# Optimization experiments

Measured on AMD Instinct MI355X. Metric: run time of the kernel, lower is better.

Reference implementation:

```python
import jax, jax.numpy as jnp
import numpy as np

STDDEV = 0.1  # matches Regularizer(stddev=0.1)


def setup_inputs() -> dict:
    key = jax.random.key(0)
    k1, k2, k3, k4 = jax.random.split(key, 4)
    B, S, D = 2048, 256, 128  # batch, num_samples, n_input
    return {
        "x": jax.random.normal(k1, (B, D), dtype=jnp.float32),
        "noise": jax.random.normal(k2, (B, S, D), dtype=jnp.float32),
        "W": jax.random.normal(k3, (D, 1), dtype=jnp.float32) * 0.1,  # inner model weight
        "b": jax.random.normal(k4, (1,), dtype=jnp.float32),          # inner model bias
    }


def reference(x, noise, W, b):
    B, S, D = noise.shape
    # neighborhood: x repeated + Gaussian noise, plus constant column -> [B, S, D+1]
    xl_feat = x[:, None, :] + noise * STDDEV                      # [B, S, D]
    ones = jnp.ones((B, S, 1), dtype=x.dtype)
    xl = jnp.concatenate([xl_feat, ones], axis=-1)                # [B, S, D+1]

    # inner model (linear + sigmoid classifier) evaluated on the neighborhood
    y = jax.nn.sigmoid(xl_feat @ W + b)                           # [B, S, 1]

    # local least-squares fit: Beta = (X^T X)^{-1} X^T y, batched over B
    XtX = jnp.einsum('bsi,bsj->bij', xl, xl)                      # [B, D+1, D+1]
    Xty = jnp.einsum('bsi,bsk->bik', xl, y)                       # [B, D+1, 1]
    Beta = jnp.linalg.solve(XtX, Xty)                             # [B, D+1, 1]

    # linear predictions -> sigmoid -> BCE(target = model output)
    y_lin = jnp.einsum('bsi,bik->bsk', xl, Beta)                  # [B, S, 1]
    logp = jax.nn.log_sigmoid(y_lin)
    log1mp = jax.nn.log_sigmoid(-y_lin)
    bce = -(y * logp + (1.0 - y) * log1mp)                        # [B, S, 1]
    # mean over stacked per-sample BCE means == global mean (equal sizes)
    return jnp.mean(bce)
```

## Files before the change

### kernel.cpp

```cpp
#include <hip/hip_runtime.h>
#include <math.h>

#define NB 2048
#define NS 256
#define ND 128
#define NCOL 129
#define LDA 132
#define TS 32
#define XTP 40
#define BSTRIDE 132
#define STDDEV 0.1f

typedef __attribute__((ext_vector_type(8))) short bf16x8;
typedef __attribute__((ext_vector_type(4))) float f32x4;

__device__ inline unsigned short f32_to_bf16_rn(float f) {
  unsigned int u = __float_as_uint(f);
  unsigned int r = (u + 0x7FFFu + ((u >> 16) & 1u)) >> 16;
  return (unsigned short)r;
}
__device__ inline float bf16u_to_f32(unsigned short h) {
  return __uint_as_float(((unsigned int)h) << 16);
}
__device__ inline float rdlane(float v, int lane) {
  return __int_as_float(__builtin_amdgcn_readlane(__float_as_int(v), lane));
}

#define FOR_ROW(F, i) F(i,0) F(i,1) F(i,2) F(i,3) F(i,4) F(i,5) F(i,6) F(i,7)
#define FOR_ALL(F) FOR_ROW(F,0) FOR_ROW(F,1) FOR_ROW(F,2) FOR_ROW(F,3) \
                   FOR_ROW(F,4) FOR_ROW(F,5) FOR_ROW(F,6) FOR_ROW(F,7)

#define ACC_DECL(i,j) float a##i##_##j = 0.f;
#define ACC_UPD(i,j)  a##i##_##j = fmaf(-m##i, rc##j, a##i##_##j);

#define ACC8(cc, c, m) \
  a##cc##_0 = fmaf(-(m), a##c##_0, a##cc##_0); \
  a##cc##_1 = fmaf(-(m), a##c##_1, a##cc##_1); \
  a##cc##_2 = fmaf(-(m), a##c##_2, a##cc##_2); \
  a##cc##_3 = fmaf(-(m), a##c##_3, a##cc##_3); \
  a##cc##_4 = fmaf(-(m), a##c##_4, a##cc##_4); \
  a##cc##_5 = fmaf(-(m), a##c##_5, a##cc##_5); \
  a##cc##_6 = fmaf(-(m), a##c##_6, a##cc##_6); \
  a##cc##_7 = fmaf(-(m), a##c##_7, a##cc##_7);

#define PF_U(c, cc) { const float m_ = pv##cc * pinv; \
  ACC8(cc, c, m_) \
  rh##cc = fmaf(-m_, rh##c, rh##cc); \
  bc##cc = fmaf(-m_, bc##c, bc##cc); }

#define PF_STEP(c, J0, J1, J2, J3, UPDS) { \
  const float pv0 = rdlane(a##c##_##J0, lsrc0); \
  const float pv1 = rdlane(a##c##_##J1, lsrc0); \
  const float pv2 = rdlane(a##c##_##J2, lsrc0); \
  const float pv3 = rdlane(a##c##_##J3, lsrc0); \
  const float pv4 = rdlane(a##c##_##J0, lsrc1); \
  const float pv5 = rdlane(a##c##_##J1, lsrc1); \
  const float pv6 = rdlane(a##c##_##J2, lsrc1); \
  const float pv7 = rdlane(a##c##_##J3, lsrc1); \
  const float pinv = 1.0f / pv##c; \
  if (tx == 3) pdiag[p8 + (c)] = pinv; \
  const float mb_ = bc##c * pinv; \
  cornb = fmaf(-mb_, bc##c, cornb); \
  cornr = fmaf(-mb_, rh##c, cornr); \
  UPDS }

#define PUBROW(c) \
  *(float4*)&rbp[(c) * LDA + txc0] = make_float4(a##c##_0, a##c##_1, a##c##_2, a##c##_3); \
  *(float4*)&rbp[(c) * LDA + txc1] = make_float4(a##c##_4, a##c##_5, a##c##_6, a##c##_7);

#define TRAIL_C(c) { \
  const float4 o0_ = *(const float4*)&rbp[(c) * LDA + ty8]; \
  const float4 o1_ = *(const float4*)&rbp[(c) * LDA + ty8 + 4]; \
  const float4 c0_ = *(const float4*)&rbp[(c) * LDA + txc0]; \
  const float4 c1_ = *(const float4*)&rbp[(c) * LDA + txc1]; \
  const float pk_ = pd[(c)]; \
  const float m0 = o0_.x*pk_, m1 = o0_.y*pk_, m2 = o0_.z*pk_, m3 = o0_.w*pk_; \
  const float m4 = o1_.x*pk_, m5 = o1_.y*pk_, m6 = o1_.z*pk_, m7 = o1_.w*pk_; \
  const float rc0 = c0_.x, rc1 = c0_.y, rc2 = c0_.z, rc3 = c0_.w; \
  const float rc4 = c1_.x, rc5 = c1_.y, rc6 = c1_.z, rc7 = c1_.w; \
  FOR_ALL(ACC_UPD) \
  hr0 = fmaf(m0, rp[(c)], hr0); hr1 = fmaf(m1, rp[(c)], hr1); \
  hr2 = fmaf(m2, rp[(c)], hr2); hr3 = fmaf(m3, rp[(c)], hr3); \
  hr4 = fmaf(m4, rp[(c)], hr4); hr5 = fmaf(m5, rp[(c)], hr5); \
  hr6 = fmaf(m6, rp[(c)], hr6); hr7 = fmaf(m7, rp[(c)], hr7); \
  hb0 = fmaf(m0, bp[(c)], hb0); hb1 = fmaf(m1, bp[(c)], hb1); \
  hb2 = fmaf(m2, bp[(c)], hb2); hb3 = fmaf(m3, bp[(c)], hb3); \
  hb4 = fmaf(m4, bp[(c)], hb4); hb5 = fmaf(m5, bp[(c)], hb5); \
  hb6 = fmaf(m6, bp[(c)], hb6); hb7 = fmaf(m7, bp[(c)], hb7); }

#define PC_U(cc, J, SRC, bev) { const float u_ = rdlane(a##cc##_##J, SRC); \
  rh##cc = fmaf(-u_, bev, rh##cc); }
#define PC_S(c, UPDS) { be##c = rh##c * pd##c; UPDS }

#define PCT_ROW(i) const float ps##i = hi \
  ? fmaf(a##i##_4, be0, fmaf(a##i##_5, be1, fmaf(a##i##_6, be2, a##i##_7 * be3))) \
  : fmaf(a##i##_0, be0, fmaf(a##i##_1, be1, fmaf(a##i##_2, be2, a##i##_3 * be3)));

#define FOR_J(F) F(0) F(1) F(2) F(3) F(4) F(5) F(6) F(7)
#define CB_DECL(j) f32x4 cb0_##j = {0.f,0.f,0.f,0.f}; f32x4 cb1_##j = {0.f,0.f,0.f,0.f};

#define MF_J(j) { \
  const bf16x8 Bh = *(const bf16x8*)&XTh[(16*(j) + tx)*XTP + kq]; \
  const bf16x8 Bl = *(const bf16x8*)&XTl[(16*(j) + tx)*XTP + kq]; \
  cb0_##j = __builtin_amdgcn_mfma_f32_16x16x32_bf16(Ah0, Bh, cb0_##j, 0,0,0); \
  cb0_##j = __builtin_amdgcn_mfma_f32_16x16x32_bf16(Ah0, Bl, cb0_##j, 0,0,0); \
  cb0_##j = __builtin_amdgcn_mfma_f32_16x16x32_bf16(Al0, Bh, cb0_##j, 0,0,0); \
  cb1_##j = __builtin_amdgcn_mfma_f32_16x16x32_bf16(Ah1, Bh, cb1_##j, 0,0,0); \
  cb1_##j = __builtin_amdgcn_mfma_f32_16x16x32_bf16(Ah1, Bl, cb1_##j, 0,0,0); \
  cb1_##j = __builtin_amdgcn_mfma_f32_16x16x32_bf16(Al1, Bh, cb1_##j, 0,0,0); }

#define TCONV(u, HV, LV, e) { \
  const float xf_ = sA[(sh + (u)) * LDA + d]; \
  const unsigned short hh_ = f32_to_bf16_rn(xf_); \
  const float hf_ = bf16u_to_f32(hh_); \
  const unsigned short ll_ = f32_to_bf16_rn(xf_ - hf_); \
  HV[e] = (short)hh_; LV[e] = (short)ll_; }

#define STAGE_IT(it, nv) { \
  const int idx_ = t + (it) * 256; \
  const int s_ = idx_ >> 5, d4_ = idx_ & 31; \
  const float4 xq_ = *(const float4*)&xv[d4_ * 4]; \
  float4 xl_; \
  xl_.x = xq_.x + STDDEV * nv.x; \
  xl_.y = xq_.y + STDDEV * nv.y; \
  xl_.z = xq_.z + STDDEV * nv.z; \
  xl_.w = xq_.w + STDDEV * nv.w; \
  *(float4*)&sA[s_ * LDA + d4_ * 4] = xl_; }

#define BW_BJ(b, j) \
  myband[(16*(b) + q4 + 0)*132 + 16*(j) + tx] = cb##b##_##j[0]; \
  myband[(16*(b) + q4 + 1)*132 + 16*(j) + tx] = cb##b##_##j[1]; \
  myband[(16*(b) + q4 + 2)*132 + 16*(j) + tx] = cb##b##_##j[2]; \
  myband[(16*(b) + q4 + 3)*132 + 16*(j) + tx] = cb##b##_##j[3];
#define BW_ALL \
  BW_BJ(0,0) BW_BJ(0,1) BW_BJ(0,2) BW_BJ(0,3) BW_BJ(0,4) BW_BJ(0,5) BW_BJ(0,6) BW_BJ(0,7) \
  BW_BJ(1,0) BW_BJ(1,1) BW_BJ(1,2) BW_BJ(1,3) BW_BJ(1,4) BW_BJ(1,5) BW_BJ(1,6) BW_BJ(1,7)
#define BR_ROW(i) { \
  const float4 lo_ = *(const float4*)&myband[(q8 + (i))*132 + txc0]; \
  const float4 hi_ = *(const float4*)&myband[(q8 + (i))*132 + txc1]; \
  a##i##_0 = lo_.x; a##i##_1 = lo_.y; a##i##_2 = lo_.z; a##i##_3 = lo_.w; \
  a##i##_4 = hi_.x; a##i##_5 = hi_.y; a##i##_6 = hi_.z; a##i##_7 = hi_.w; }
#define BR_ALL \
  BR_ROW(0) BR_ROW(1) BR_ROW(2) BR_ROW(3) BR_ROW(4) BR_ROW(5) BR_ROW(6) BR_ROW(7)

__global__ __launch_bounds__(256, 2)
void k_fit(const float* __restrict__ x, const float* __restrict__ noise,
           const float* __restrict__ W, const float* __restrict__ bptr,
           float* __restrict__ Beta) {
  __shared__ __align__(16) float region0[9344];
  __shared__ __align__(16) float rbuf[2 * 8 * LDA];
  __shared__ __align__(16) float pdiag[NCOL + 3];
  __shared__ __align__(16) float bcol[NCOL + 3];
  __shared__ __align__(16) float rhs[NCOL + 3];
  __shared__ __align__(16) float betaL[NCOL + 3];
  __shared__ __align__(16) float yt[TS];
  __shared__ __align__(16) float Wl[128];
  __shared__ __align__(16) float xv[128];
  __shared__ __align__(16) float sp0[ND], sp1[ND];

  float* sA = region0;
  unsigned short* XTh = (unsigned short*)(region0 + 4224);
  unsigned short* XTl = (unsigned short*)(region0 + 4224 + 2560);
  float* band = region0;

  const int t  = threadIdx.x;
  const int b  = blockIdx.x;
  const int tx = t & 15;
  const int ty = t >> 4;
  const int wv = t >> 6;
  const int txc0 = tx * 4;
  const int txc1 = 64 + tx * 4;
  const int ty8 = ty * 8;
  const int q4 = 4 * (ty & 3);
  const int q8 = 8 * (ty & 3);
  const int kq = 8 * (ty & 3);
  const float bscal = bptr[0];

  if (t < 128) { Wl[t] = W[t]; xv[t] = x[(size_t)b * ND + t]; }

  FOR_J(CB_DECL)
  float col_acc = 0.f, xty_acc = 0.f;

  const float* nbase = noise + (size_t)b * (NS * ND);

  float4 nv0, nv1, nv2, nv3;
  {
    const float4* src = (const float4*)nbase;
    nv0 = src[t]; nv1 = src[t + 256]; nv2 = src[t + 512]; nv3 = src[t + 768];
  }

  for (int s0 = 0; s0 < NS; s0 += TS) {
    __syncthreads();
    {
      STAGE_IT(0, nv0) STAGE_IT(1, nv1) STAGE_IT(2, nv2) STAGE_IT(3, nv3)
      if (t < TS) sA[t * LDA + ND] = 1.0f;
    }
    if (s0 + TS < NS) {
      const float4* src = (const float4*)(nbase + (size_t)(s0 + TS) * ND);
      nv0 = src[t]; nv1 = src[t + 256]; nv2 = src[t + 512]; nv3 = src[t + 768];
    }
    __syncthreads();
    {
      const int d = t >> 1;
      const int sh = (t & 1) * 16;
      bf16x8 h0, h1, l0, l1;
      TCONV(0,h0,l0,0) TCONV(1,h0,l0,1) TCONV(2,h0,l0,2) TCONV(3,h0,l0,3)
      TCONV(4,h0,l0,4) TCONV(5,h0,l0,5) TCONV(6,h0,l0,6) TCONV(7,h0,l0,7)
      TCONV(8,h1,l1,0) TCONV(9,h1,l1,1) TCONV(10,h1,l1,2) TCONV(11,h1,l1,3)
      TCONV(12,h1,l1,4) TCONV(13,h1,l1,5) TCONV(14,h1,l1,6) TCONV(15,h1,l1,7)
      *(bf16x8*)&XTh[d * XTP + sh]     = h0;
      *(bf16x8*)&XTh[d * XTP + sh + 8] = h1;
      *(bf16x8*)&XTl[d * XTP + sh]     = l0;
      *(bf16x8*)&XTl[d * XTP + sh + 8] = l1;
    }
    {
      int sl = t >> 3, p = t & 7;
      float acw = 0.f;
#pragma unroll
      for (int d = 0; d < 4; ++d) {
        float4 a = *(const float4*)&sA[sl * LDA + p * 16 + d * 4];
        float4 w = *(const float4*)&Wl[p * 16 + d * 4];
        acw += a.x * w.x + a.y * w.y + a.z * w.z + a.w * w.w;
      }
      acw += __shfl_xor(acw, 1);
      acw += __shfl_xor(acw, 2);
      acw += __shfl_xor(acw, 4);
      if (p == 0) yt[sl] = 1.f / (1.f + expf(-(acw + bscal)));
    }
    __syncthreads();
    if (t < NCOL) {
      for (int s = 0; s < TS; ++s) {
        float v = sA[s * LDA + t];
        col_acc += v;
        xty_acc += yt[s] * v;
      }
    }
    {
      const bf16x8 Ah0 = *(const bf16x8*)&XTh[(32*wv + tx)*XTP + kq];
      const bf16x8 Al0 = *(const bf16x8*)&XTl[(32*wv + tx)*XTP + kq];
      const bf16x8 Ah1 = *(const bf16x8*)&XTh[(32*wv + 16 + tx)*XTP + kq];
      const bf16x8 Al1 = *(const bf16x8*)&XTl[(32*wv + 16 + tx)*XTP + kq];
      MF_J(0) MF_J(1) MF_J(2) MF_J(3) MF_J(4) MF_J(5) MF_J(6) MF_J(7)
    }
  }
  if (t < NCOL) { bcol[t] = col_acc; rhs[t] = xty_acc; }
  __syncthreads();

  FOR_ALL(ACC_DECL)
  {
    float* myband = band + (wv & 1) * 4224;
    if (wv < 2) {
      BW_ALL
      asm volatile("s_waitcnt lgkmcnt(0)" ::: "memory");
      BR_ALL
      asm volatile("s_waitcnt lgkmcnt(0)" ::: "memory");
    }
    __syncthreads();
    if (wv >= 2) {
      BW_ALL
      asm volatile("s_waitcnt lgkmcnt(0)" ::: "memory");
      BR_ALL
      asm volatile("s_waitcnt lgkmcnt(0)" ::: "memory");
    }
    __syncthreads();
  }

#pragma unroll 1
  for (int p = 0; p < 16; ++p) {
    const int p8 = p * 8;
    const int ol = (p < 8) ? (p << 1) : ((p - 8) << 1);
    float* rbp = &rbuf[(p & 1) * (8 * LDA)];
    if (ty == p) {
      asm volatile("s_waitcnt lgkmcnt(0)" ::: "memory");
      const float4 rq0 = *(const float4*)&rhs[p8];
      const float4 rq1 = *(const float4*)&rhs[p8 + 4];
      const float4 bq0 = *(const float4*)&bcol[p8];
      const float4 bq1 = *(const float4*)&bcol[p8 + 4];
      float rh0 = rq0.x, rh1 = rq0.y, rh2 = rq0.z, rh3 = rq0.w;
      float rh4 = rq1.x, rh5 = rq1.y, rh6 = rq1.z, rh7 = rq1.w;
      float bc0 = bq0.x, bc1 = bq0.y, bc2 = bq0.z, bc3 = bq0.w;
      float bc4 = bq1.x, bc5 = bq1.y, bc6 = bq1.z, bc7 = bq1.w;
      float cornr = rhs[ND], cornb = bcol[ND];
      const int lsrc0 = ((p & 3) << 4) + ol;
      const int lsrc1 = lsrc0 + 1;
      if (p < 8) {
        PF_STEP(0, 0,1,2,3, PF_U(0,1) PF_U(0,2) PF_U(0,3) PF_U(0,4) PF_U(0,5) PF_U(0,6) PF_U(0,7))
        PF_STEP(1, 0,1,2,3, PF_U(1,2) PF_U(1,3) PF_U(1,4) PF_U(1,5) PF_U(1,6) PF_U(1,7))
        PF_STEP(2, 0,1,2,3, PF_U(2,3) PF_U(2,4) PF_U(2,5) PF_U(2,6) PF_U(2,7))
        PF_STEP(3, 0,1,2,3, PF_U(3,4) PF_U(3,5) PF_U(3,6) PF_U(3,7))
        PF_STEP(4, 0,1,2,3, PF_U(4,5) PF_U(4,6) PF_U(4,7))
        PF_STEP(5, 0,1,2,3, PF_U(5,6) PF_U(5,7))
        PF_STEP(6, 0,1,2,3, PF_U(6,7))
        PF_STEP(7, 0,1,2,3, )
      } else {
        PF_STEP(0, 4,5,6,7, PF_U(0,1) PF_U(0,2) PF_U(0,3) PF_U(0,4) PF_U(0,5) PF_U(0,6) PF_U(0,7))
        PF_STEP(1, 4,5,6,7, PF_U(1,2) PF_U(1,3) PF_U(1,4) PF_U(1,5) PF_U(1,6) PF_U(1,7))
        PF_STEP(2, 4,5,6,7, PF_U(2,3) PF_U(2,4) PF_U(2,5) PF_U(2,6) PF_U(2,7))
        PF_STEP(3, 4,5,6,7, PF_U(3,4) PF_U(3,5) PF_U(3,6) PF_U(3,7))
        PF_STEP(4, 4,5,6,7, PF_U(4,5) PF_U(4,6) PF_U(4,7))
        PF_STEP(5, 4,5,6,7, PF_U(5,6) PF_U(5,7))
        PF_STEP(6, 4,5,6,7, PF_U(6,7))
        PF_STEP(7, 4,5,6,7, )
      }
      PUBROW(0) PUBROW(1) PUBROW(2) PUBROW(3)
      PUBROW(4) PUBROW(5) PUBROW(6) PUBROW(7)
      if (tx == 0) {
        *(float4*)&rhs[p8]     = make_float4(rh0, rh1, rh2, rh3);
        *(float4*)&rhs[p8 + 4] = make_float4(rh4, rh5, rh6, rh7);
      }
      if (tx == 1) {
        *(float4*)&bcol[p8]     = make_float4(bc0, bc1, bc2, bc3);
        *(float4*)&bcol[p8 + 4] = make_float4(bc4, bc5, bc6, bc7);
      }
      if (tx == 2) { rhs[ND] = cornr; bcol[ND] = cornb; }
    }
    __syncthreads();
    if (ty > p) {
      const float4 d0_ = *(const float4*)&pdiag[p8];
      const float4 d1_ = *(const float4*)&pdiag[p8 + 4];
      const float4 rq0_ = *(const float4*)&rhs[p8];
      const float4 rq1_ = *(const float4*)&rhs[p8 + 4];
      const float4 bq0_ = *(const float4*)&bcol[p8];
      const float4 bq1_ = *(const float4*)&bcol[p8 + 4];
      const float pd[8] = {d0_.x, d0_.y, d0_.z, d0_.w, d1_.x, d1_.y, d1_.z, d1_.w};
      const float rp[8] = {rq0_.x, rq0_.y, rq0_.z, rq0_.w, rq1_.x, rq1_.y, rq1_.z, rq1_.w};
      const float bp[8] = {bq0_.x, bq0_.y, bq0_.z, bq0_.w, bq1_.x, bq1_.y, bq1_.z, bq1_.w};
      float hr0 = 0.f, hr1 = 0.f, hr2 = 0.f, hr3 = 0.f;
      float hr4 = 0.f, hr5 = 0.f, hr6 = 0.f, hr7 = 0.f;
      float hb0 = 0.f, hb1 = 0.f, hb2 = 0.f, hb3 = 0.f;
      float hb4 = 0.f, hb5 = 0.f, hb6 = 0.f, hb7 = 0.f;
      TRAIL_C(0) TRAIL_C(1) TRAIL_C(2) TRAIL_C(3)
      TRAIL_C(4) TRAIL_C(5) TRAIL_C(6) TRAIL_C(7)
      if (tx == 0) {
        float4 h0 = *(float4*)&rhs[ty8]; float4 h1 = *(float4*)&rhs[ty8 + 4];
        h0.x -= hr0; h0.y -= hr1; h0.z -= hr2; h0.w -= hr3;
        h1.x -= hr4; h1.y -= hr5; h1.z -= hr6; h1.w -= hr7;
        *(float4*)&rhs[ty8] = h0; *(float4*)&rhs[ty8 + 4] = h1;
      }
      if (tx == 1) {
        float4 h0 = *(float4*)&bcol[ty8]; float4 h1 = *(float4*)&bcol[ty8 + 4];
        h0.x -= hb0; h0.y -= hb1; h0.z -= hb2; h0.w -= hb3;
        h1.x -= hb4; h1.y -= hb5; h1.z -= hb6; h1.w -= hb7;
        *(float4*)&bcol[ty8] = h0; *(float4*)&bcol[ty8 + 4] = h1;
      }
    }
  }
  __syncthreads();

  if (t == 0) betaL[ND] = rhs[ND] / bcol[ND];
  if (t < ND) { sp0[t] = 0.f; sp1[t] = 0.f; }
  __syncthreads();
  if (t < ND) rhs[t] = fmaf(-bcol[t], betaL[ND], rhs[t]);
  __syncthreads();
#pragma unroll 1
  for (int p = 15; p >= 0; --p) {
    const int p8 = p * 8;
    const bool hi = (p >= 8);
    const int ol = hi ? ((p - 8) << 1) : (p << 1);
    const int txo0 = ol, txo1 = ol + 1;
    if (ty == p) {
      asm volatile("s_waitcnt lgkmcnt(0)" ::: "memory");
      const float4 rq0 = *(const float4*)&rhs[p8];
      const float4 rq1 = *(const float4*)&rhs[p8 + 4];
      const float4 sq0 = *(const float4*)&sp0[p8];
      const float4 sq1 = *(const float4*)&sp0[p8 + 4];
      const float4 uq0 = *(const float4*)&sp1[p8];
      const float4 uq1 = *(const float4*)&sp1[p8 + 4];
      const float4 dq0 = *(const float4*)&pdiag[p8];
      const float4 dq1 = *(const float4*)&pdiag[p8 + 4];
      float rh0 = rq0.x - sq0.x - uq0.x, rh1 = rq0.y - sq0.y - uq0.y;
      float rh2 = rq0.z - sq0.z - uq0.z, rh3 = rq0.w - sq0.w - uq0.w;
      float rh4 = rq1.x - sq1.x - uq1.x, rh5 = rq1.y - sq1.y - uq1.y;
      float rh6 = rq1.z - sq1.z - uq1.z, rh7 = rq1.w - sq1.w - uq1.w;
      const float pd0 = dq0.x, pd1 = dq0.y, pd2 = dq0.z, pd3 = dq0.w;
      const float pd4 = dq1.x, pd5 = dq1.y, pd6 = dq1.z, pd7 = dq1.w;
      const int lsrc0 = ((p & 3) << 4) + ol;
      const int lsrc1 = lsrc0 + 1;
      float be0, be1, be2, be3, be4, be5, be6, be7;
      if (p < 8) {
        PC_S(7, PC_U(0,3,lsrc1,be7) PC_U(1,3,lsrc1,be7) PC_U(2,3,lsrc1,be7) PC_U(3,3,lsrc1,be7) PC_U(4,3,lsrc1,be7) PC_U(5,3,lsrc1,be7) PC_U(6,3,lsrc1,be7))
        PC_S(6, PC_U(0,2,lsrc1,be6) PC_U(1,2,lsrc1,be6) PC_U(2,2,lsrc1,be6) PC_U(3,2,lsrc1,be6) PC_U(4,2,lsrc1,be6) PC_U(5,2,lsrc1,be6))
        PC_S(5, PC_U(0,1,lsrc1,be5) PC_U(1,1,lsrc1,be5) PC_U(2,1,lsrc1,be5) PC_U(3,1,lsrc1,be5) PC_U(4,1,lsrc1,be5))
        PC_S(4, PC_U(0,0,lsrc1,be4) PC_U(1,0,lsrc1,be4) PC_U(2,0,lsrc1,be4) PC_U(3,0,lsrc1,be4))
        PC_S(3, PC_U(0,3,lsrc0,be3) PC_U(1,3,lsrc0,be3) PC_U(2,3,lsrc0,be3))
        PC_S(2, PC_U(0,2,lsrc0,be2) PC_U(1,2,lsrc0,be2))
        PC_S(1, PC_U(0,1,lsrc0,be1))
        PC_S(0, )
      } else {
        PC_S(7, PC_U(0,7,lsrc1,be7) PC_U(1,7,lsrc1,be7) PC_U(2,7,lsrc1,be7) PC_U(3,7,lsrc1,be7) PC_U(4,7,lsrc1,be7) PC_U(5,7,lsrc1,be7) PC_U(6,7,lsrc1,be7))
        PC_S(6, PC_U(0,6,lsrc1,be6) PC_U(1,6,lsrc1,be6) PC_U(2,6,lsrc1,be6) PC_U(3,6,lsrc1,be6) PC_U(4,6,lsrc1,be6) PC_U(5,6,lsrc1,be6))
        PC_S(5, PC_U(0,5,lsrc1,be5) PC_U(1,5,lsrc1,be5) PC_U(2,5,lsrc1,be5) PC_U(3,5,lsrc1,be5) PC_U(4,5,lsrc1,be5))
        PC_S(4, PC_U(0,4,lsrc1,be4) PC_U(1,4,lsrc1,be4) PC_U(2,4,lsrc1,be4) PC_U(3,4,lsrc1,be4))
        PC_S(3, PC_U(0,7,lsrc0,be3) PC_U(1,7,lsrc0,be3) PC_U(2,7,lsrc0,be3))
        PC_S(2, PC_U(0,6,lsrc0,be2) PC_U(1,6,lsrc0,be2))
        PC_S(1, PC_U(0,5,lsrc0,be1))
        PC_S(0, )
      }
      if (tx == 0) {
        *(float4*)&betaL[p8]     = make_float4(be0, be1, be2, be3);
        *(float4*)&betaL[p8 + 4] = make_float4(be4, be5, be6, be7);
      }
    }
    __syncthreads();
    if (ty < p && (tx == txo0 || tx == txo1)) {
      const bool second = (tx == txo1);
      const float4 beq = *(const float4*)&betaL[p8 + (second ? 4 : 0)];
      float* spd = second ? sp1 : sp0;
      const float be0 = beq.x, be1 = beq.y, be2 = beq.z, be3 = beq.w;
      PCT_ROW(0) PCT_ROW(1) PCT_ROW(2) PCT_ROW(3)
      PCT_ROW(4) PCT_ROW(5) PCT_ROW(6) PCT_ROW(7)
      float4 h0 = *(float4*)&spd[ty8]; float4 h1 = *(float4*)&spd[ty8 + 4];
      h0.x += ps0; h0.y += ps1; h0.z += ps2; h0.w += ps3;
      h1.x += ps4; h1.y += ps5; h1.z += ps6; h1.w += ps7;
      *(float4*)&spd[ty8] = h0; *(float4*)&spd[ty8 + 4] = h1;
    }
    __syncthreads();
  }
  if (t < NCOL) Beta[(size_t)b * BSTRIDE + t] = betaL[t];
}

__device__ inline float logsig(float v) {
  if (v >= 0.f) return -log1pf(expf(-v));
  return v - log1pf(expf(v));
}

__global__ __launch_bounds__(256)
void k_bce(const float* __restrict__ x, const float* __restrict__ noise,
           const float* __restrict__ W, const float* __restrict__ bptr,
           const float* __restrict__ Beta, float* __restrict__ partial) {
  const int t    = threadIdx.x;
  const int lane = t & 31;
  const size_t grp = ((size_t)blockIdx.x * 256 + t) >> 5;
  const float bscal = bptr[0];
  const float4 w4 = *((const float4*)W + lane);

  float lsum = 0.f;
  size_t base = grp * 8;
  for (int it = 0; it < 8; ++it) {
    size_t idx = base + it;
    int bb = (int)(idx >> 8);
    float4 n4 = *((const float4*)noise + idx * 32 + lane);
    float4 x4 = *((const float4*)x + (size_t)bb * 32 + lane);
    float4 p4 = *((const float4*)(Beta + (size_t)bb * BSTRIDE) + lane);
    float4 xl;
    xl.x = x4.x + STDDEV * n4.x;
    xl.y = x4.y + STDDEV * n4.y;
    xl.z = x4.z + STDDEV * n4.z;
    xl.w = x4.w + STDDEV * n4.w;
    float aw = xl.x * w4.x + xl.y * w4.y + xl.z * w4.z + xl.w * w4.w;
    float ab = xl.x * p4.x + xl.y * p4.y + xl.z * p4.z + xl.w * p4.w;
#pragma unroll
    for (int off = 16; off >= 1; off >>= 1) {
      aw += __shfl_xor(aw, off);
      ab += __shfl_xor(ab, off);
    }
    if (lane == 0) {
      float y    = 1.f / (1.f + expf(-(aw + bscal)));
      float ylin = ab + Beta[(size_t)bb * BSTRIDE + 128];
      float lp   = logsig(ylin);
      float lmp  = logsig(-ylin);
      lsum += -(y * lp + (1.f - y) * lmp);
    }
  }
  lsum += __shfl_xor(lsum, 32);
  __shared__ float red[4];
  if ((t & 63) == 0) red[t >> 6] = lsum;
  __syncthreads();
  if (t == 0) partial[blockIdx.x] = red[0] + red[1] + red[2] + red[3];
}

__global__ void k_final(const float* __restrict__ partial, float* __restrict__ out,
                        int n, float inv) {
  __shared__ float red[256];
  float s = 0.f;
  for (int i = threadIdx.x; i < n; i += 256) s += partial[i];
  red[threadIdx.x] = s;
  __syncthreads();
  for (int k = 128; k > 0; k >>= 1) {
    if (threadIdx.x < k) red[threadIdx.x] += red[threadIdx.x + k];
    __syncthreads();
  }
  if (threadIdx.x == 0) out[0] = red[0] * inv;
}

extern "C" void kernel_launch(void* const* d_in, const int* in_sizes, int n_in,
                              void* d_out, int out_size, void* d_ws, size_t ws_size,
                              hipStream_t stream) {
  const float* x     = (const float*)d_in[0];
  const float* noise = (const float*)d_in[1];
  const float* W     = (const float*)d_in[2];
  const float* bptr  = (const float*)d_in[3];
  float* out = (float*)d_out;

  float* Beta = (float*)d_ws;
  const size_t beta_bytes = (size_t)NB * BSTRIDE * sizeof(float);
  float* partial = (float*)((char*)d_ws + ((beta_bytes + 255) & ~(size_t)255));

  const int nblk2 = (NB * NS) / (8 * 8);

  k_fit<<<NB, 256, 0, stream>>>(x, noise, W, bptr, Beta);
  k_bce<<<nblk2, 256, 0, stream>>>(x, noise, W, bptr, Beta, partial);
  k_final<<<1, 256, 0, stream>>>(partial, out, nblk2, 1.0f / (float)(NB * NS));
}
```

Measured before the change: 455.1 us.

## Alias k_fit scratch buffers into shared region for 3 blocks/CU; restructure k_bce

In k_fit, the separate rbuf and sp0/sp1 shared arrays are removed and aliased into the existing region0 buffer. The launch bound is raised from 2 to 3 blocks per multiprocessor, so less LDS per block allows higher occupancy. k_bce now maps one block to 64 samples of a single batch row, hoisting the x and Beta loads out of the loop and doing the sigmoid/BCE math in parallel across 64 threads via shared memory instead of serially on lane 0. Risks include aliasing hazards if region0 is live while rbuf/sp are used, and register pressure under the tighter launch bound.

```diff
diff --git a/kernel.cpp b/kernel.cpp
--- a/kernel.cpp
+++ b/kernel.cpp
@@ -143,12 +143,11 @@
 #define BR_ALL \
   BR_ROW(0) BR_ROW(1) BR_ROW(2) BR_ROW(3) BR_ROW(4) BR_ROW(5) BR_ROW(6) BR_ROW(7)
 
-__global__ __launch_bounds__(256, 2)
+__global__ __launch_bounds__(256, 3)
 void k_fit(const float* __restrict__ x, const float* __restrict__ noise,
            const float* __restrict__ W, const float* __restrict__ bptr,
            float* __restrict__ Beta) {
   __shared__ __align__(16) float region0[9344];
-  __shared__ __align__(16) float rbuf[2 * 8 * LDA];
   __shared__ __align__(16) float pdiag[NCOL + 3];
   __shared__ __align__(16) float bcol[NCOL + 3];
   __shared__ __align__(16) float rhs[NCOL + 3];
@@ -156,12 +155,14 @@
   __shared__ __align__(16) float yt[TS];
   __shared__ __align__(16) float Wl[128];
   __shared__ __align__(16) float xv[128];
-  __shared__ __align__(16) float sp0[ND], sp1[ND];
 
   float* sA = region0;
   unsigned short* XTh = (unsigned short*)(region0 + 4224);
   unsigned short* XTl = (unsigned short*)(region0 + 4224 + 2560);
   float* band = region0;
+  float* rbuf = region0;
+  float* sp0  = region0 + 2112;
+  float* sp1  = region0 + 2240;
 
   const int t  = threadIdx.x;
   const int b  = blockIdx.x;
@@ -430,18 +431,18 @@
            const float* __restrict__ Beta, float* __restrict__ partial) {
   const int t    = threadIdx.x;
   const int lane = t & 31;
-  const size_t grp = ((size_t)blockIdx.x * 256 + t) >> 5;
-  const float bscal = bptr[0];
+  const int grp  = t >> 5;
+  const int bb   = blockIdx.x >> 2;
+  const size_t sbase = (size_t)blockIdx.x * 64;
+  __shared__ float saw[64], sab[64];
+
   const float4 w4 = *((const float4*)W + lane);
-
-  float lsum = 0.f;
-  size_t base = grp * 8;
+  const float4 x4 = *((const float4*)x + (size_t)bb * 32 + lane);
+  const float4 p4 = *((const float4*)(Beta + (size_t)bb * BSTRIDE) + lane);
+
   for (int it = 0; it < 8; ++it) {
-    size_t idx = base + it;
-    int bb = (int)(idx >> 8);
+    const size_t idx = sbase + grp * 8 + it;
     float4 n4 = *((const float4*)noise + idx * 32 + lane);
-    float4 x4 = *((const float4*)x + (size_t)bb * 32 + lane);
-    float4 p4 = *((const float4*)(Beta + (size_t)bb * BSTRIDE) + lane);
     float4 xl;
     xl.x = x4.x + STDDEV * n4.x;
     xl.y = x4.y + STDDEV * n4.y;
@@ -454,19 +455,19 @@
       aw += __shfl_xor(aw, off);
       ab += __shfl_xor(ab, off);
     }
-    if (lane == 0) {
-      float y    = 1.f / (1.f + expf(-(aw + bscal)));
-      float ylin = ab + Beta[(size_t)bb * BSTRIDE + 128];
-      float lp   = logsig(ylin);
-      float lmp  = logsig(-ylin);
-      lsum += -(y * lp + (1.f - y) * lmp);
-    }
-  }
-  lsum += __shfl_xor(lsum, 32);
-  __shared__ float red[4];
-  if ((t & 63) == 0) red[t >> 6] = lsum;
+    if (lane == 0) { saw[grp * 8 + it] = aw; sab[grp * 8 + it] = ab; }
+  }
   __syncthreads();
-  if (t == 0) partial[blockIdx.x] = red[0] + red[1] + red[2] + red[3];
+  if (t < 64) {
+    const float bscal = bptr[0];
+    const float beta128 = Beta[(size_t)bb * BSTRIDE + 128];
+    const float y    = 1.f / (1.f + expf(-(saw[t] + bscal)));
+    const float ylin = sab[t] + beta128;
+    float v = -(y * logsig(ylin) + (1.f - y) * logsig(-ylin));
+#pragma unroll
+    for (int off = 32; off >= 1; off >>= 1) v += __shfl_xor(v, off);
+    if (t == 0) partial[blockIdx.x] = v;
+  }
 }
 
 __global__ void k_final(const float* __restrict__ partial, float* __restrict__ out,
@@ -496,7 +497,7 @@
   const size_t beta_bytes = (size_t)NB * BSTRIDE * sizeof(float);
   float* partial = (float*)((char*)d_ws + ((beta_bytes + 255) & ~(size_t)255));
 
-  const int nblk2 = (NB * NS) / (8 * 8);
+  const int nblk2 = (NB * NS) / 64;
 
   k_fit<<<NB, 256, 0, stream>>>(x, noise, W, bptr, Beta);
   k_bce<<<nblk2, 256, 0, stream>>>(x, noise, W, bptr, Beta, partial);
```

After: 731.7 us. 1.61x slower.
